# Kernel optimization log

Hardware: AMD Instinct MI355X
Metric: run time of the kernel (lower is better)

## Reference

```python
import jax, jax.numpy as jnp
import numpy as np

D_MODEL = 1024
N_HEAD = 16
DK = D_MODEL // N_HEAD
D_FF = 2048
EPS = 1e-6
NEG = -1e10


def layer_norm(x, gamma, beta):
    # torch .std() is unbiased (N-1), and eps is added to std (not var)
    mean = jnp.mean(x, axis=-1, keepdims=True)
    var = jnp.sum((x - mean) ** 2, axis=-1, keepdims=True) / (x.shape[-1] - 1)
    std = jnp.sqrt(var)
    return gamma * (x - mean) / (std + EPS) + beta


def setup_inputs() -> dict:
    key = jax.random.key(0)
    ks = jax.random.split(key, 12)
    s = 0.02
    inp = {
        'x': jax.random.normal(ks[0], (16, 512, D_MODEL), dtype=jnp.float32),
        'x_mask': jax.random.randint(ks[1], (16, 1, 1, 512), 0, 2, dtype=jnp.int32),
        'Wq': jax.random.normal(ks[2], (D_MODEL, D_MODEL), dtype=jnp.float32) * s,
        'bq': jnp.zeros((D_MODEL,), jnp.float32),
        'Wk': jax.random.normal(ks[3], (D_MODEL, D_MODEL), dtype=jnp.float32) * s,
        'bk': jnp.zeros((D_MODEL,), jnp.float32),
        'Wv': jax.random.normal(ks[4], (D_MODEL, D_MODEL), dtype=jnp.float32) * s,
        'bv': jnp.zeros((D_MODEL,), jnp.float32),
        'Wo': jax.random.normal(ks[5], (D_MODEL, D_MODEL), dtype=jnp.float32) * s,
        'bo': jnp.zeros((D_MODEL,), jnp.float32),
        'gamma1': jnp.ones((D_MODEL,), jnp.float32),
        'beta1': jnp.zeros((D_MODEL,), jnp.float32),
        'W1': jax.random.normal(ks[6], (D_MODEL, D_FF), dtype=jnp.float32) * s,
        'b1': jnp.zeros((D_FF,), jnp.float32),
        'W2': jax.random.normal(ks[7], (D_FF, D_MODEL), dtype=jnp.float32) * s,
        'b2': jnp.zeros((D_MODEL,), jnp.float32),
        'gamma2': jnp.ones((D_MODEL,), jnp.float32),
        'beta2': jnp.zeros((D_MODEL,), jnp.float32),
    }
    return inp


def reference(x, x_mask, Wq, bq, Wk, bk, Wv, bv, Wo, bo, gamma1, beta1,
              W1, b1, W2, b2, gamma2, beta2):
    B, S, _ = x.shape
    # QKV projections -> [B, S, H, DK]
    q = (x @ Wq + bq).reshape(B, S, N_HEAD, DK)
    k = (x @ Wk + bk).reshape(B, S, N_HEAD, DK)
    v = (x @ Wv + bv).reshape(B, S, N_HEAD, DK)
    # scores [B, H, Sq, Sk]
    scores = jnp.einsum('bqhd,bkhd->bhqk', q, k) / jnp.sqrt(jnp.float32(DK))
    scores = jnp.where(x_mask == 0, jnp.float32(NEG), scores)
    probs = jax.nn.softmax(scores, axis=-1)
    attn = jnp.einsum('bhqk,bkhd->bqhd', probs, v).reshape(B, S, D_MODEL)
    attn_out = attn @ Wo + bo
    # residual + post-LN 1
    h = layer_norm(attn_out + x, gamma1, beta1)
    # FFN (exact GELU as torch nn.GELU default)
    ffn = jax.nn.gelu(h @ W1 + b1, approximate=False) @ W2 + b2
    out = layer_norm(ffn + h, gamma2, beta2)
    return out
```

## Files before the change

### kernel.cpp

```cpp
#include <hip/hip_runtime.h>
#include <math.h>

#define B_ 16
#define S_ 512
#define DM 1024
#define NH 16
#define DFF 2048

typedef short bf16x8 __attribute__((ext_vector_type(8)));
typedef float f32x4 __attribute__((ext_vector_type(4)));
typedef unsigned short u16;

__device__ __forceinline__ u16 f2bf(float f) {
  unsigned int u = __float_as_uint(f);
  u += 0x7FFF + ((u >> 16) & 1);
  return (u16)(u >> 16);
}

__device__ __forceinline__ float bf2f(u16 u) {
  return __uint_as_float(((unsigned)u) << 16);
}

__device__ __forceinline__ unsigned cvtpk_bf16(float lo, float hi) {
  unsigned r;
  asm("v_cvt_pk_bf16_f32 %0, %1, %2" : "=v"(r) : "v"(lo), "v"(hi));
  return r;
}

__device__ __forceinline__ float gelu_exact(float x) {
  return 0.5f * x * (1.0f + erff(x * 0.70710678118654752f));
}

__device__ __forceinline__ void gload_lds16(const void* g, void* l) {
  __builtin_amdgcn_global_load_lds((const __attribute__((address_space(1))) void*)g,
                                   (__attribute__((address_space(3))) void*)l, 16, 0, 0);
}

#define QSCALE 0.18033688011112042f
#define MASKNEG -1.442695e10f

__global__ __launch_bounds__(256)
void prep_all(const float* __restrict__ Wq, const float* __restrict__ Wk,
              const float* __restrict__ Wv, const float* __restrict__ Wo,
              const float* __restrict__ W1, const float* __restrict__ W2,
              u16* __restrict__ wqkvt, u16* __restrict__ wot,
              u16* __restrict__ w1t, u16* __restrict__ w2t,
              const float* __restrict__ bq, const float* __restrict__ bk,
              const float* __restrict__ bv, float* __restrict__ bqkv,
              const float* __restrict__ x, u16* __restrict__ xb) {
  const int bid = blockIdx.x;
  if (bid >= 8204) {
    int i = ((bid - 8204) * 256 + threadIdx.x) * 4;
    float4 v = *(const float4*)(x + i);
    uint2 pk;
    pk.x = (unsigned)f2bf(v.x) | ((unsigned)f2bf(v.y) << 16);
    pk.y = (unsigned)f2bf(v.z) | ((unsigned)f2bf(v.w) << 16);
    *(uint2*)(xb + i) = pk;
    return;
  }
  if (bid >= 8192) {
    int i = (bid - 8192) * 256 + threadIdx.x;
    bqkv[i] = (i < 1024) ? bq[i] : ((i < 2048) ? bk[i - 1024] : bv[i - 2048]);
    return;
  }
  const float* W;
  u16* Wt;
  int K, N, bx, by;
  if (bid < 4096) {
    const int m = bid >> 10, t = bid & 1023;
    K = 1024; N = 1024; bx = t & 31; by = t >> 5;
    W = (m == 0) ? Wq : (m == 1) ? Wk : (m == 2) ? Wv : Wo;
    Wt = (m == 3) ? wot : wqkvt + m * 1048576;
  } else if (bid < 6144) {
    const int t = bid - 4096;
    K = 1024; N = 2048; bx = t & 63; by = t >> 6; W = W1; Wt = w1t;
  } else {
    const int t = bid - 6144;
    K = 2048; N = 1024; bx = t & 31; by = t >> 5; W = W2; Wt = w2t;
  }
  __shared__ float tile[32][33];
  const int n0 = bx * 32, k0 = by * 32;
  const int tx = threadIdx.x & 31, ty = threadIdx.x >> 5;
#pragma unroll
  for (int j = 0; j < 32; j += 8)
    tile[ty + j][tx] = W[(size_t)(k0 + ty + j) * N + n0 + tx];
  __syncthreads();
#pragma unroll
  for (int j = 0; j < 32; j += 8)
    Wt[(size_t)(n0 + ty + j) * K + k0 + tx] = f2bf(tile[tx][ty + j]);
}

template <int EPI>
__global__ __launch_bounds__(256, 2)
void gemm_mfma(const u16* __restrict__ A, const u16* __restrict__ Bt,
               const float* __restrict__ bias, void* __restrict__ Cout,
               u16* __restrict__ vT, int M, int N, int K) {
  __shared__ __align__(16) char lds[73728];
  const int tid = threadIdx.x;
  const int w = tid >> 6, lane = tid & 63;
  const int wm = w >> 1, wn = w & 1;

  const int gx = gridDim.x;
  const int nwg = gx * gridDim.y;
  const int lin = blockIdx.y * gx + blockIdx.x;
  const int wg = (lin & 7) * (nwg >> 3) + (lin >> 3);
  const int bm = wg / gx, bn = wg % gx;

  const int NT = K >> 5;

  const int srow = w * 16 + (lane >> 2);
  const int skel = ((lane & 3) ^ (lane >> 4)) * 8;
  const u16* gA = A + (size_t)(bm * 256 + srow) * K + skel;
  const u16* gB = Bt + (size_t)(bn * 128 + srow) * K + skel;
  const size_t rs64 = (size_t)64 * K;
  const int dstb = w * 1024;

  const int lr = lane & 15, kg = lane >> 4;
  const int kslot = (kg ^ ((lr >> 2) & 3)) << 4;
  const int fAoff = (wm * 128 + lr) * 64 + kslot;
  const int fBoff = 16384 + (wn * 64 + lr) * 64 + kslot;

  f32x4 acc[8][4];
#pragma unroll
  for (int i = 0; i < 8; ++i)
#pragma unroll
    for (int j = 0; j < 4; ++j) acc[i][j] = (f32x4){0.f, 0.f, 0.f, 0.f};

#define STAGE_A(t_, sl_)                                         \
  do {                                                           \
    const u16* g_ = gA + (size_t)(t_) * 32;                      \
    char* d_ = lds + (sl_) * 24576 + dstb;                       \
    gload_lds16(g_, d_);                                         \
    gload_lds16(g_ + rs64, d_ + 4096);                           \
    gload_lds16(g_ + 2 * rs64, d_ + 8192);                       \
    gload_lds16(g_ + 3 * rs64, d_ + 12288);                      \
  } while (0)
#define STAGE_B(t_, sl_)                                         \
  do {                                                           \
    const u16* g_ = gB + (size_t)(t_) * 32;                      \
    char* d_ = lds + (sl_) * 24576 + 16384 + dstb;               \
    gload_lds16(g_, d_);                                         \
    gload_lds16(g_ + rs64, d_ + 4096);                           \
  } while (0)

  STAGE_A(0, 0);
  STAGE_B(0, 0);
  STAGE_A(1, 1);
  STAGE_B(1, 1);
  asm volatile("s_waitcnt vmcnt(6)" ::: "memory");
  __builtin_amdgcn_s_barrier();
  __builtin_amdgcn_sched_barrier(0);

  int cs = 0, ss = 2;
  for (int t = 0; t < NT; ++t) {
    const int st = (t + 2 < NT) ? (t + 2) : (NT - 1);
    const char* fA = lds + cs * 24576 + fAoff;
    const char* fB = lds + cs * 24576 + fBoff;
    bf16x8 av[4], bv[4];
#pragma unroll
    for (int mi = 0; mi < 4; ++mi) av[mi] = *(const bf16x8*)(fA + mi * 1024);
#pragma unroll
    for (int ni = 0; ni < 4; ++ni) bv[ni] = *(const bf16x8*)(fB + ni * 1024);
    STAGE_A(st, ss);
    __builtin_amdgcn_s_setprio(1);
#pragma unroll
    for (int mi = 0; mi < 4; ++mi)
#pragma unroll
      for (int ni = 0; ni < 4; ++ni)
        acc[mi][ni] = __builtin_amdgcn_mfma_f32_16x16x32_bf16(av[mi], bv[ni], acc[mi][ni], 0, 0, 0);
    __builtin_amdgcn_s_setprio(0);
    bf16x8 av2[4];
#pragma unroll
    for (int mi = 0; mi < 4; ++mi) av2[mi] = *(const bf16x8*)(fA + 4096 + mi * 1024);
    STAGE_B(st, ss);
    __builtin_amdgcn_s_setprio(1);
#pragma unroll
    for (int mi = 0; mi < 4; ++mi)
#pragma unroll
      for (int ni = 0; ni < 4; ++ni)
        acc[4 + mi][ni] = __builtin_amdgcn_mfma_f32_16x16x32_bf16(av2[mi], bv[ni], acc[4 + mi][ni], 0, 0, 0);
    __builtin_amdgcn_s_setprio(0);
    asm volatile("s_waitcnt vmcnt(6) lgkmcnt(0)" ::: "memory");
    __builtin_amdgcn_s_barrier();
    __builtin_amdgcn_sched_barrier(0);
    cs = (cs == 2) ? 0 : cs + 1;
    ss = (ss == 2) ? 0 : ss + 1;
  }
#undef STAGE_A
#undef STAGE_B

  const int crow0 = bm * 256 + wm * 128;
  const int ccol0 = bn * 128 + wn * 64;
#pragma unroll
  for (int mi = 0; mi < 8; ++mi) {
#pragma unroll
    for (int ni = 0; ni < 4; ++ni) {
      const int col = ccol0 + ni * 16 + lr;
      const float bv_ = bias[col];
      const int rowb = crow0 + mi * 16 + (lane >> 4) * 4;
      float v[4];
#pragma unroll
      for (int r = 0; r < 4; ++r) v[r] = acc[mi][ni][r] + bv_;
      if (EPI == 1) {
#pragma unroll
        for (int r = 0; r < 4; ++r)
          ((u16*)Cout)[(size_t)(rowb + r) * N + col] = f2bf(gelu_exact(v[r]));
      } else if (EPI == 2) {
#pragma unroll
        for (int r = 0; r < 4; ++r)
          ((float*)Cout)[(size_t)(rowb + r) * N + col] = v[r];
      } else if (EPI == 4) {
#pragma unroll
        for (int r = 0; r < 4; ++r)
          ((u16*)Cout)[(size_t)(rowb + r) * N + col] = f2bf(v[r]);
      } else {
        if (col < 2048) {
          const float sc = (col < 1024) ? QSCALE : 1.0f;
#pragma unroll
          for (int r = 0; r < 4; ++r)
            ((u16*)Cout)[(size_t)(rowb + r) * 2048 + col] = f2bf(v[r] * sc);
        } else {
          const int b = rowb >> 9, s = rowb & 511;
          const int hd = col - 2048;
          ushort4 pk;
          pk.x = f2bf(v[0]); pk.y = f2bf(v[1]); pk.z = f2bf(v[2]); pk.w = f2bf(v[3]);
          *(ushort4*)(vT + ((size_t)(b * NH + (hd >> 6)) * 64 + (hd & 63)) * S_ + s) = pk;
        }
      }
    }
  }
}

__global__ __launch_bounds__(256, 3)
void attn_kernel(const u16* __restrict__ qk,
                 const u16* __restrict__ vT,
                 const int* __restrict__ mask,
                 u16* __restrict__ out) {
  __shared__ __align__(16) u16 Qs[32 * 72];
  __shared__ __align__(16) u16 Pl[32 * 520];
  __shared__ __align__(16) float Mlf[512];
  __shared__ __align__(16) float Rsum[32][4];

  const int tid = threadIdx.x;
  const int w = tid >> 6, lane = tid & 63;
  const int bid = blockIdx.x;
  const int widx = (bid & 7) * 512 + (bid >> 3);
  const int qt = widx & 15, h = (widx >> 4) & 15, b = widx >> 8;
  const int q0 = qt * 32;
  const int arow = lane & 15, kg = lane >> 4;

  {
    int r = tid >> 3, slot = tid & 7;
    bf16x8 v = *(const bf16x8*)(qk + (size_t)(b * S_ + q0 + r) * 2048 + h * 64 + slot * 8);
    *(bf16x8*)((char*)Qs + r * 144 + slot * 16) = v;
  }
  Mlf[tid] = (mask[b * S_ + tid] == 0) ? MASKNEG : 0.f;
  Mlf[tid + 256] = (mask[b * S_ + tid + 256] == 0) ? MASKNEG : 0.f;

  const u16* vb = vT + ((size_t)(b * NH + h) * 64 + w * 16 + arow) * S_ + kg * 8;
  bf16x8 vv[8];
#pragma unroll
  for (int i = 0; i < 8; ++i) vv[i] = *(const bf16x8*)(vb + i * 32);

  __syncthreads();

  bf16x8 qf[2][2];
#pragma unroll
  for (int mi = 0; mi < 2; ++mi)
#pragma unroll
    for (int kk = 0; kk < 2; ++kk)
      qf[mi][kk] = *(const bf16x8*)((char*)Qs + (mi * 16 + arow) * 144 + kk * 64 + kg * 16);

  f32x4 s0[8], s1[8];
  const u16* kbase = qk + (size_t)(b * S_) * 2048 + 1024 + h * 64 + kg * 8;
#pragma unroll
  for (int half = 0; half < 2; ++half) {
    bf16x8 kvl[4][2];
#pragma unroll
    for (int j = 0; j < 4; ++j) {
      const int colg = w * 128 + (half * 4 + j) * 16 + arow;
      const u16* kr = kbase + (size_t)colg * 2048;
      kvl[j][0] = *(const bf16x8*)(kr);
      kvl[j][1] = *(const bf16x8*)(kr + 32);
    }
#pragma unroll
    for (int j = 0; j < 4; ++j) {
      const int ni = half * 4 + j;
      f32x4 a0 = {0.f, 0.f, 0.f, 0.f}, a1 = {0.f, 0.f, 0.f, 0.f};
      a0 = __builtin_amdgcn_mfma_f32_16x16x32_bf16(kvl[j][0], qf[0][0], a0, 0, 0, 0);
      a0 = __builtin_amdgcn_mfma_f32_16x16x32_bf16(kvl[j][1], qf[0][1], a0, 0, 0, 0);
      a1 = __builtin_amdgcn_mfma_f32_16x16x32_bf16(kvl[j][0], qf[1][0], a1, 0, 0, 0);
      a1 = __builtin_amdgcn_mfma_f32_16x16x32_bf16(kvl[j][1], qf[1][1], a1, 0, 0, 0);
      const f32x4 mb = *(const f32x4*)&Mlf[w * 128 + ni * 16 + kg * 4];
      s0[ni] = a0 + mb;
      s1[ni] = a1 + mb;
    }
  }

  f32x4 ac0 = {0.f, 0.f, 0.f, 0.f}, ac1 = ac0;
#pragma unroll
  for (int ni = 0; ni < 8; ++ni) {
#pragma unroll
    for (int r = 0; r < 4; ++r) {
      s0[ni][r] = __builtin_amdgcn_exp2f(s0[ni][r]);
      s1[ni][r] = __builtin_amdgcn_exp2f(s1[ni][r]);
    }
    ac0 += s0[ni];
    ac1 += s1[ni];
  }
  float t0 = ac0[0] + ac0[1] + ac0[2] + ac0[3];
  float t1 = ac1[0] + ac1[1] + ac1[2] + ac1[3];
  t0 += __shfl_xor(t0, 16);
  t0 += __shfl_xor(t0, 32);
  t1 += __shfl_xor(t1, 16);
  t1 += __shfl_xor(t1, 32);
  if (kg == 0) {
    Rsum[arow][w] = t0;
    Rsum[16 + arow][w] = t1;
  }

  {
    const int kq = w * 128 + kg * 4;
    char* const p0 = (char*)Pl + (arow * 520 + kq) * 2;
    char* const p1 = (char*)Pl + ((16 + arow) * 520 + kq) * 2;
#pragma unroll
    for (int ni = 0; ni < 8; ++ni) {
      uint2 pk;
      pk.x = cvtpk_bf16(s0[ni][0], s0[ni][1]);
      pk.y = cvtpk_bf16(s0[ni][2], s0[ni][3]);
      *(uint2*)(p0 + ni * 32) = pk;
      pk.x = cvtpk_bf16(s1[ni][0], s1[ni][1]);
      pk.y = cvtpk_bf16(s1[ni][2], s1[ni][3]);
      *(uint2*)(p1 + ni * 32) = pk;
    }
  }
  __syncthreads();

  {
    f32x4 oa[2];
    oa[0] = (f32x4){0.f, 0.f, 0.f, 0.f};
    oa[1] = (f32x4){0.f, 0.f, 0.f, 0.f};
#pragma unroll
    for (int t16 = 0; t16 < 16; ++t16) {
      const int sk0 = t16 * 32;
      bf16x8 bfr = (t16 < 8) ? vv[t16] : *(const bf16x8*)(vb + t16 * 32);
#pragma unroll
      for (int mi = 0; mi < 2; ++mi) {
        bf16x8 pa = *(const bf16x8*)(Pl + (mi * 16 + arow) * 520 + sk0 + kg * 8);
        oa[mi] = __builtin_amdgcn_mfma_f32_16x16x32_bf16(pa, bfr, oa[mi], 0, 0, 0);
      }
    }
#pragma unroll
    for (int mi = 0; mi < 2; ++mi)
#pragma unroll
      for (int r = 0; r < 4; ++r) {
        const int rloc = mi * 16 + kg * 4 + r;
        f32x4 sv = *(const f32x4*)&Rsum[rloc][0];
        const float inv = 1.0f / (sv[0] + sv[1] + sv[2] + sv[3]);
        const int qrow = q0 + rloc;
        out[(size_t)(b * S_ + qrow) * DM + h * 64 + w * 16 + arow] = f2bf(oa[mi][r] * inv);
      }
  }
}

template <int AB, int RB, int WF, int WB>
__global__ __launch_bounds__(256)
void ln_kernel(const void* __restrict__ a, const void* __restrict__ res,
               const float* __restrict__ gamma, const float* __restrict__ beta,
               float* __restrict__ outf, u16* __restrict__ outb) {
  const int row = blockIdx.x, tid = threadIdx.x;
  const int w = tid >> 6, lane = tid & 63;
  const size_t base = (size_t)row * DM + tid * 4;
  float v0, v1, v2, v3;
  {
    float a0, a1, a2, a3, r0, r1, r2, r3;
    if (AB) {
      ushort4 u = *(const ushort4*)((const u16*)a + base);
      a0 = bf2f(u.x); a1 = bf2f(u.y); a2 = bf2f(u.z); a3 = bf2f(u.w);
    } else {
      float4 u = *(const float4*)((const float*)a + base);
      a0 = u.x; a1 = u.y; a2 = u.z; a3 = u.w;
    }
    if (RB) {
      ushort4 u = *(const ushort4*)((const u16*)res + base);
      r0 = bf2f(u.x); r1 = bf2f(u.y); r2 = bf2f(u.z); r3 = bf2f(u.w);
    } else {
      float4 u = *(const float4*)((const float*)res + base);
      r0 = u.x; r1 = u.y; r2 = u.z; r3 = u.w;
    }
    v0 = a0 + r0; v1 = a1 + r1; v2 = a2 + r2; v3 = a3 + r3;
  }
  float s = v0 + v1 + v2 + v3;
  float ss = v0 * v0 + v1 * v1 + v2 * v2 + v3 * v3;
#pragma unroll
  for (int off = 32; off >= 1; off >>= 1) {
    s += __shfl_down(s, off);
    ss += __shfl_down(ss, off);
  }
  __shared__ float ps[4], pss[4], mb[2];
  if (lane == 0) { ps[w] = s; pss[w] = ss; }
  __syncthreads();
  if (tid == 0) {
    float S = ps[0] + ps[1] + ps[2] + ps[3];
    float SS = pss[0] + pss[1] + pss[2] + pss[3];
    float mean = S * (1.0f / DM);
    float var = (SS - (float)DM * mean * mean) * (1.0f / (DM - 1));
    var = fmaxf(var, 0.f);
    mb[0] = mean;
    mb[1] = 1.0f / (sqrtf(var) + 1e-6f);
  }
  __syncthreads();
  const float mean = mb[0], rinv = mb[1];
  const int c = tid * 4;
  float y0 = gamma[c] * (v0 - mean) * rinv + beta[c];
  float y1 = gamma[c + 1] * (v1 - mean) * rinv + beta[c + 1];
  float y2 = gamma[c + 2] * (v2 - mean) * rinv + beta[c + 2];
  float y3 = gamma[c + 3] * (v3 - mean) * rinv + beta[c + 3];
  if (WF) {
    float4 o = {y0, y1, y2, y3};
    *(float4*)(outf + base) = o;
  }
  if (WB) {
    uint2 pk;
    pk.x = (unsigned)f2bf(y0) | ((unsigned)f2bf(y1) << 16);
    pk.y = (unsigned)f2bf(y2) | ((unsigned)f2bf(y3) << 16);
    *(uint2*)(outb + base) = pk;
  }
}


extern "C" void kernel_launch(void* const* d_in, const int* in_sizes, int n_in,
                              void* d_out, int out_size, void* d_ws, size_t ws_size,
                              hipStream_t stream) {
  const float* x = (const float*)d_in[0];
  const int* xm = (const int*)d_in[1];
  const float* Wq = (const float*)d_in[2];
  const float* bq = (const float*)d_in[3];
  const float* Wk = (const float*)d_in[4];
  const float* bk = (const float*)d_in[5];
  const float* Wv = (const float*)d_in[6];
  const float* bv = (const float*)d_in[7];
  const float* Wo = (const float*)d_in[8];
  const float* bo = (const float*)d_in[9];
  const float* g1 = (const float*)d_in[10];
  const float* be1 = (const float*)d_in[11];
  const float* W1 = (const float*)d_in[12];
  const float* b1 = (const float*)d_in[13];
  const float* W2 = (const float*)d_in[14];
  const float* b2 = (const float*)d_in[15];
  const float* g2 = (const float*)d_in[16];
  const float* be2 = (const float*)d_in[17];

  char* ws = (char*)d_ws;
  u16* xb = (u16*)(ws);
  u16* wqkvt = (u16*)(ws + 16777216);
  u16* wot = (u16*)(ws + 23068672);
  u16* w1t = (u16*)(ws + 25165824);
  u16* w2t = (u16*)(ws + 29360128);
  float* bqkv = (float*)(ws + 33554432);
  u16* qkb = (u16*)(ws + 33566720);
  u16* vtb = (u16*)(ws + 67121152);
  u16* attnb = (u16*)(ws + 83898368);
  u16* attnpb = (u16*)(ws + 100675584);
  u16* f2b = (u16*)(ws + 117452800);
  u16* hb = (u16*)(ws + 134230016);

  prep_all<<<dim3(16396), dim3(256), 0, stream>>>(Wq, Wk, Wv, Wo, W1, W2,
                                                  wqkvt, wot, w1t, w2t,
                                                  bq, bk, bv, bqkv, x, xb);

  gemm_mfma<3><<<dim3(24, 32), dim3(256), 0, stream>>>(xb, wqkvt, bqkv, (void*)qkb, vtb, 8192, 3072, 1024);
  attn_kernel<<<dim3(4096), dim3(256), 0, stream>>>(qkb, vtb, xm, attnb);
  gemm_mfma<4><<<dim3(8, 32), dim3(256), 0, stream>>>(attnb, wot, bo, (void*)attnpb, (u16*)nullptr, 8192, 1024, 1024);
  ln_kernel<1, 1, 0, 1><<<dim3(8192), dim3(256), 0, stream>>>(attnpb, xb, g1, be1, (float*)nullptr, hb);
  gemm_mfma<1><<<dim3(16, 32), dim3(256), 0, stream>>>(hb, w1t, b1, (void*)qkb, (u16*)nullptr, 8192, 2048, 1024);
  gemm_mfma<4><<<dim3(8, 32), dim3(256), 0, stream>>>(qkb, w2t, b2, (void*)f2b, (u16*)nullptr, 8192, 1024, 2048);
  ln_kernel<1, 1, 1, 0><<<dim3(8192), dim3(256), 0, stream>>>(f2b, hb, g2, be2, (float*)d_out, (u16*)nullptr);
}
```

Baseline: 287.2 us.

## Split GEMM workgroup into 8 waves with 64x64 per-wave tiles

The MFMA GEMM now runs 512 threads (8 waves) per workgroup instead of 256. Each wave owns a 64x64 output sub-tile, down from 128x64, which halves the accumulator registers per wave. The cooperative global-to-LDS staging is rewritten so each thread issues three loads per k-step (two for A, one for B), with the wait counts and pipeline adjusted to match. The aim is more waves in flight to hide memory and LDS latency. In exchange, each wave reuses fewer LDS fragments per MFMA and barrier synchronisation grows across more waves; the launch bound of 4 blocks may also be unattainable given the 72KB LDS per block.

```diff
diff --git a/kernel.cpp b/kernel.cpp
--- a/kernel.cpp
+++ b/kernel.cpp
@@ -91,7 +91,7 @@
 }
 
 template <int EPI>
-__global__ __launch_bounds__(256, 2)
+__global__ __launch_bounds__(512, 4)
 void gemm_mfma(const u16* __restrict__ A, const u16* __restrict__ Bt,
                const float* __restrict__ bias, void* __restrict__ Cout,
                u16* __restrict__ vT, int M, int N, int K) {
@@ -108,46 +108,37 @@
 
   const int NT = K >> 5;
 
-  const int srow = w * 16 + (lane >> 2);
-  const int skel = ((lane & 3) ^ (lane >> 4)) * 8;
+  const int srow = tid >> 2;
+  const int skel = ((lane & 3) ^ ((lane >> 4) & 3)) * 8;
   const u16* gA = A + (size_t)(bm * 256 + srow) * K + skel;
   const u16* gB = Bt + (size_t)(bn * 128 + srow) * K + skel;
-  const size_t rs64 = (size_t)64 * K;
+  const size_t rs128 = (size_t)128 * K;
   const int dstb = w * 1024;
 
   const int lr = lane & 15, kg = lane >> 4;
   const int kslot = (kg ^ ((lr >> 2) & 3)) << 4;
-  const int fAoff = (wm * 128 + lr) * 64 + kslot;
+  const int fAoff = (wm * 64 + lr) * 64 + kslot;
   const int fBoff = 16384 + (wn * 64 + lr) * 64 + kslot;
 
-  f32x4 acc[8][4];
-#pragma unroll
-  for (int i = 0; i < 8; ++i)
+  f32x4 acc[4][4];
+#pragma unroll
+  for (int i = 0; i < 4; ++i)
 #pragma unroll
     for (int j = 0; j < 4; ++j) acc[i][j] = (f32x4){0.f, 0.f, 0.f, 0.f};
 
-#define STAGE_A(t_, sl_)                                         \
+#define STAGE_T(t_, sl_)                                         \
   do {                                                           \
-    const u16* g_ = gA + (size_t)(t_) * 32;                      \
+    const u16* ga_ = gA + (size_t)(t_) * 32;                     \
+    const u16* gb_ = gB + (size_t)(t_) * 32;                     \
     char* d_ = lds + (sl_) * 24576 + dstb;                       \
-    gload_lds16(g_, d_);                                         \
-    gload_lds16(g_ + rs64, d_ + 4096);                           \
-    gload_lds16(g_ + 2 * rs64, d_ + 8192);                       \
-    gload_lds16(g_ + 3 * rs64, d_ + 12288);                      \
+    gload_lds16(ga_, d_);                                        \
+    gload_lds16(ga_ + rs128, d_ + 8192);                         \
+    gload_lds16(gb_, d_ + 16384);                                \
   } while (0)
-#define STAGE_B(t_, sl_)                                         \
-  do {                                                           \
-    const u16* g_ = gB + (size_t)(t_) * 32;                      \
-    char* d_ = lds + (sl_) * 24576 + 16384 + dstb;               \
-    gload_lds16(g_, d_);                                         \
-    gload_lds16(g_ + rs64, d_ + 4096);                           \
-  } while (0)
-
-  STAGE_A(0, 0);
-  STAGE_B(0, 0);
-  STAGE_A(1, 1);
-  STAGE_B(1, 1);
-  asm volatile("s_waitcnt vmcnt(6)" ::: "memory");
+
+  STAGE_T(0, 0);
+  STAGE_T(1, 1);
+  asm volatile("s_waitcnt vmcnt(3)" ::: "memory");
   __builtin_amdgcn_s_barrier();
   __builtin_amdgcn_sched_barrier(0);
 
@@ -161,7 +152,7 @@
     for (int mi = 0; mi < 4; ++mi) av[mi] = *(const bf16x8*)(fA + mi * 1024);
 #pragma unroll
     for (int ni = 0; ni < 4; ++ni) bv[ni] = *(const bf16x8*)(fB + ni * 1024);
-    STAGE_A(st, ss);
+    STAGE_T(st, ss);
     __builtin_amdgcn_s_setprio(1);
 #pragma unroll
     for (int mi = 0; mi < 4; ++mi)
@@ -169,30 +160,18 @@
       for (int ni = 0; ni < 4; ++ni)
         acc[mi][ni] = __builtin_amdgcn_mfma_f32_16x16x32_bf16(av[mi], bv[ni], acc[mi][ni], 0, 0, 0);
     __builtin_amdgcn_s_setprio(0);
-    bf16x8 av2[4];
-#pragma unroll
-    for (int mi = 0; mi < 4; ++mi) av2[mi] = *(const bf16x8*)(fA + 4096 + mi * 1024);
-    STAGE_B(st, ss);
-    __builtin_amdgcn_s_setprio(1);
-#pragma unroll
-    for (int mi = 0; mi < 4; ++mi)
-#pragma unroll
-      for (int ni = 0; ni < 4; ++ni)
-        acc[4 + mi][ni] = __builtin_amdgcn_mfma_f32_16x16x32_bf16(av2[mi], bv[ni], acc[4 + mi][ni], 0, 0, 0);
-    __builtin_amdgcn_s_setprio(0);
-    asm volatile("s_waitcnt vmcnt(6) lgkmcnt(0)" ::: "memory");
+    asm volatile("s_waitcnt vmcnt(3) lgkmcnt(0)" ::: "memory");
     __builtin_amdgcn_s_barrier();
     __builtin_amdgcn_sched_barrier(0);
     cs = (cs == 2) ? 0 : cs + 1;
     ss = (ss == 2) ? 0 : ss + 1;
   }
-#undef STAGE_A
-#undef STAGE_B
-
-  const int crow0 = bm * 256 + wm * 128;
+#undef STAGE_T
+
+  const int crow0 = bm * 256 + wm * 64;
   const int ccol0 = bn * 128 + wn * 64;
 #pragma unroll
-  for (int mi = 0; mi < 8; ++mi) {
+  for (int mi = 0; mi < 4; ++mi) {
 #pragma unroll
     for (int ni = 0; ni < 4; ++ni) {
       const int col = ccol0 + ni * 16 + lr;
@@ -469,11 +448,11 @@
                                                   wqkvt, wot, w1t, w2t,
                                                   bq, bk, bv, bqkv, x, xb);
 
-  gemm_mfma<3><<<dim3(24, 32), dim3(256), 0, stream>>>(xb, wqkvt, bqkv, (void*)qkb, vtb, 8192, 3072, 1024);
+  gemm_mfma<3><<<dim3(24, 32), dim3(512), 0, stream>>>(xb, wqkvt, bqkv, (void*)qkb, vtb, 8192, 3072, 1024);
   attn_kernel<<<dim3(4096), dim3(256), 0, stream>>>(qkb, vtb, xm, attnb);
-  gemm_mfma<4><<<dim3(8, 32), dim3(256), 0, stream>>>(attnb, wot, bo, (void*)attnpb, (u16*)nullptr, 8192, 1024, 1024);
+  gemm_mfma<4><<<dim3(8, 32), dim3(512), 0, stream>>>(attnb, wot, bo, (void*)attnpb, (u16*)nullptr, 8192, 1024, 1024);
   ln_kernel<1, 1, 0, 1><<<dim3(8192), dim3(256), 0, stream>>>(attnpb, xb, g1, be1, (float*)nullptr, hb);
-  gemm_mfma<1><<<dim3(16, 32), dim3(256), 0, stream>>>(hb, w1t, b1, (void*)qkb, (u16*)nullptr, 8192, 2048, 1024);
-  gemm_mfma<4><<<dim3(8, 32), dim3(256), 0, stream>>>(qkb, w2t, b2, (void*)f2b, (u16*)nullptr, 8192, 1024, 2048);
+  gemm_mfma<1><<<dim3(16, 32), dim3(512), 0, stream>>>(hb, w1t, b1, (void*)qkb, (u16*)nullptr, 8192, 2048, 1024);
+  gemm_mfma<4><<<dim3(8, 32), dim3(512), 0, stream>>>(qkb, w2t, b2, (void*)f2b, (u16*)nullptr, 8192, 1024, 2048);
   ln_kernel<1, 1, 1, 0><<<dim3(8192), dim3(256), 0, stream>>>(f2b, hb, g2, be2, (float*)d_out, (u16*)nullptr);
 }
```

New measurement: 285.3 us, median of 2. About the same (-0.7%).
